# Optimization experiments

Hardware: AMD Instinct MI355X
Metric: run time of the kernel (lower is better)

The kernel has to match this reference:

```python
import jax, jax.numpy as jnp
import numpy as np

N_NODES = 100000
N_EDGES = 1600000
N_FEAT = 8
N_EFEAT = 4
STATE = 32  # node_state_size
N_GEN = 10000
ITERS = 3


def _fix_max(m):
    # TF unsorted_segment_max fills empty segments with dtype.min (finite)
    return jnp.where(jnp.isneginf(m), jnp.finfo(m.dtype).min, m)


def _fix_min(m):
    return jnp.where(jnp.isposinf(m), jnp.finfo(m.dtype).max, m)


def _l2_normalize(x, eps=1e-12):
    return x * jax.lax.rsqrt(jnp.maximum(jnp.sum(x * x, axis=-1, keepdims=True), eps))


def _dense_init(key, fan_in, fan_out):
    return jax.random.normal(key, (fan_in, fan_out), jnp.float32) * (1.0 / np.sqrt(fan_in))


def setup_inputs() -> dict:
    key = jax.random.key(0)
    ks = jax.random.split(key, 12)
    x = jax.random.normal(ks[0], (N_NODES, N_FEAT), jnp.float32)
    edge_weights = jax.random.uniform(ks[1], (N_EDGES, N_EFEAT), jnp.float32)
    edges = jax.random.randint(ks[2], (2, N_EDGES), 0, N_NODES)
    generators_nodes = jax.random.randint(ks[3], (N_GEN,), 0, N_NODES)
    # update_fn: 128 -> 256 -> 128 -> 32 (tanh)
    Wu1 = _dense_init(ks[4], 4 * STATE, 256); bu1 = jnp.zeros((256,), jnp.float32)
    Wu2 = _dense_init(ks[5], 256, 128);       bu2 = jnp.zeros((128,), jnp.float32)
    Wu3 = _dense_init(ks[6], 128, STATE);     bu3 = jnp.zeros((STATE,), jnp.float32)
    # readout: 32 -> 64 -> 32 -> 1 (tanh, tanh, linear)
    Wr1 = _dense_init(ks[7], STATE, 64);      br1 = jnp.zeros((64,), jnp.float32)
    Wr2 = _dense_init(ks[8], 64, 32);         br2 = jnp.zeros((32,), jnp.float32)
    Wr3 = _dense_init(ks[9], 32, 1);          br3 = jnp.zeros((1,), jnp.float32)
    return {"x": x, "edge_weights": edge_weights,
            "Wu1": Wu1, "bu1": bu1, "Wu2": Wu2, "bu2": bu2, "Wu3": Wu3, "bu3": bu3,
            "Wr1": Wr1, "br1": br1, "Wr2": Wr2, "br2": br2, "Wr3": Wr3, "br3": br3,
            "edges": edges, "generators_nodes": generators_nodes}


def reference(x, edge_weights, Wu1, bu1, Wu2, bu2, Wu3, bu3,
              Wr1, br1, Wr2, br2, Wr3, br3, edges, generators_nodes):
    n = x.shape[0]
    node_idx, nbr_idx = edges[0], edges[1]
    ones = jnp.ones((edge_weights.shape[0], 1), x.dtype)
    cnt = jnp.maximum(jax.ops.segment_sum(ones, node_idx, num_segments=n), 1.0)  # [n,1]

    # prepare(): edge-weight stats per destination node, concat with features, pad to STATE
    w_sum = jax.ops.segment_sum(edge_weights, node_idx, num_segments=n)
    w_mean = w_sum / cnt
    w_max = _fix_max(jax.ops.segment_max(edge_weights, node_idx, num_segments=n))
    w_min = _fix_min(jax.ops.segment_min(edge_weights, node_idx, num_segments=n))
    reps = jnp.concatenate([x, w_mean, w_max, w_min, w_sum], axis=1)  # [n, 24]
    reps = jnp.pad(reps, ((0, 0), (0, STATE - reps.shape[1])))        # [n, 32]

    for _ in range(ITERS):
        msgs = jnp.take(reps, nbr_idx, axis=0)  # gather neighbour states [E, 32]
        m_mean = jax.ops.segment_sum(msgs, node_idx, num_segments=n) / cnt
        m_max = _fix_max(jax.ops.segment_max(msgs, node_idx, num_segments=n))
        m_min = _fix_min(jax.ops.segment_min(msgs, node_idx, num_segments=n))
        h = jnp.concatenate([reps, m_mean, m_max, m_min], axis=1)  # [n, 128]
        h = jnp.tanh(h @ Wu1 + bu1)
        h = jnp.tanh(h @ Wu2 + bu2)
        h = jnp.tanh(h @ Wu3 + bu3)
        reps = _l2_normalize(h)

    reps = jnp.where(jnp.isnan(reps), jnp.zeros_like(reps), reps)
    g = jnp.take(reps, generators_nodes, axis=0)  # [n_gen, 32]
    g = jnp.tanh(g @ Wr1 + br1)
    g = jnp.tanh(g @ Wr2 + br2)
    values = g @ Wr3 + br3  # linear final activation
    return values.reshape(-1)
```

## Files before the change

kernel.cpp:

```cpp
#include <hip/hip_runtime.h>
#include <cfloat>
#include <cmath>


typedef _Float16 half_t;
typedef _Float16 half8 __attribute__((ext_vector_type(8)));
typedef _Float16 half4_t __attribute__((ext_vector_type(4)));
typedef _Float16 half2_t __attribute__((ext_vector_type(2)));
typedef float f32x4 __attribute__((ext_vector_type(4)));

#define NPB 512
#define BIN_CAP 9216
#define IDXCAP 4352

__device__ __forceinline__ float fast_tanh(float x) {
    float e = __builtin_amdgcn_exp2f(x * 2.8853900817779268f);
    return 1.0f - 2.0f * __builtin_amdgcn_rcpf(1.0f + e);
}

__device__ __forceinline__ half_t cvt_clamp(float v) {
    return (half_t)fminf(fmaxf(v, -60000.f), 60000.f);
}

__device__ __forceinline__ half2_t h2shfl_xor(half2_t v, int mask) {
    int i = __builtin_bit_cast(int, v);
    i = __shfl_xor(i, mask);
    return __builtin_bit_cast(half2_t, i);
}

__global__ __launch_bounds__(256) void k_binA(
    const int* __restrict__ dst, const int* __restrict__ src,
    const float4* __restrict__ ew4,
    int* __restrict__ binCnt, int4* __restrict__ staged, int E, int nbins) {
    __shared__ int cnt[256], base[256], cur[256];
    int t = threadIdx.x;
    cnt[t] = 0;
    cur[t] = 0;
    __syncthreads();
    int e0 = blockIdx.x * 8192;
#pragma unroll 4
    for (int i = 0; i < 32; ++i) {
        int e = e0 + i * 256 + t;
        if (e < E) atomicAdd(&cnt[dst[e] >> 9], 1);
    }
    __syncthreads();
    if (t < nbins && cnt[t] > 0) base[t] = atomicAdd(&binCnt[t], cnt[t]);
    __syncthreads();
#pragma unroll 4
    for (int i = 0; i < 32; ++i) {
        int e = e0 + i * 256 + t;
        if (e < E) {
            int d = dst[e];
            int b = d >> 9;
            int j = base[b] + atomicAdd(&cur[b], 1);
            if (j < BIN_CAP) {
                float4 w = ew4[e];
                half2_t lo = {(half_t)w.x, (half_t)w.y};
                half2_t hi = {(half_t)w.z, (half_t)w.w};
                staged[(size_t)b * BIN_CAP + j] =
                    make_int4(src[e], d & (NPB - 1),
                              __builtin_bit_cast(int, lo),
                              __builtin_bit_cast(int, hi));
            }
        }
    }
}

__global__ void k_scanN(const int* __restrict__ binCnt, int* __restrict__ binStart,
                        int* __restrict__ row_start, int nbins, int n, int E) {
    __shared__ int sh[256];
    int t = threadIdx.x;
    int v = (t < nbins) ? binCnt[t] : 0;
    sh[t] = v;
    __syncthreads();
    for (int s = 1; s < 256; s <<= 1) {
        int u = (t >= s) ? sh[t - s] : 0;
        __syncthreads();
        sh[t] += u;
        __syncthreads();
    }
    if (t < nbins) binStart[t] = sh[t] - v;
    if (t == 0) row_start[n] = E;
}

__global__ __launch_bounds__(512) void k_binB(
    const int* __restrict__ binCnt, const int* __restrict__ binStart,
    const int4* __restrict__ staged, const float* __restrict__ x,
    int* __restrict__ row_start, int* __restrict__ snbr, int2* __restrict__ sew,
    half_t* __restrict__ reps, int n) {
    __shared__ int deg[NPB], cur[NPB], rsl[NPB];
    int t = threadIdx.x;
    int bin = blockIdx.x;
    int cntE = min(binCnt[bin], BIN_CAP);
    int pbase = binStart[bin];
    const int4* st = staged + (size_t)bin * BIN_CAP;

    deg[t] = 0;
    cur[t] = 0;
    __syncthreads();

    for (int i = t; i < cntE; i += 512)
        atomicAdd(&deg[st[i].y], 1);
    __syncthreads();

    int own = deg[t];
    for (int s = 1; s < NPB; s <<= 1) {
        int u = (t >= s) ? deg[t - s] : 0;
        __syncthreads();
        deg[t] += u;
        __syncthreads();
    }
    int excl = deg[t] - own;
    rsl[t] = pbase + excl;
    int node = bin * NPB + t;
    if (node < n) row_start[node] = pbase + excl;
    __syncthreads();

    for (int i = t; i < cntE; i += 512) {
        int4 v = st[i];
        int p = rsl[v.y] + atomicAdd(&cur[v.y], 1);
        snbr[p] = v.x;
        sew[p] = make_int2(v.z, v.w);
    }
    __syncthreads();

    if (node < n) {
        int base = rsl[t];
        float s0 = 0.f, s1 = 0.f, s2 = 0.f, s3 = 0.f;
        half2_t mxlo = {(half_t)-65504.f, (half_t)-65504.f};
        half2_t mxhi = mxlo;
        half2_t mnlo = {(half_t)65504.f, (half_t)65504.f};
        half2_t mnhi = mnlo;
#pragma unroll 2
        for (int k = 0; k < own; ++k) {
            int2 e = sew[base + k];
            half2_t lo = __builtin_bit_cast(half2_t, e.x);
            half2_t hi = __builtin_bit_cast(half2_t, e.y);
            s0 += (float)lo[0];
            s1 += (float)lo[1];
            s2 += (float)hi[0];
            s3 += (float)hi[1];
            mxlo = __builtin_elementwise_max(mxlo, lo);
            mxhi = __builtin_elementwise_max(mxhi, hi);
            mnlo = __builtin_elementwise_min(mnlo, lo);
            mnhi = __builtin_elementwise_min(mnhi, hi);
        }
        float cnt = fmaxf((float)own, 1.0f);
        float rc = __builtin_amdgcn_rcpf(cnt);
        float mx0, mx1, mx2, mx3, mn0, mn1, mn2, mn3;
        if (own == 0) {
            mx0 = mx1 = mx2 = mx3 = -FLT_MAX;
            mn0 = mn1 = mn2 = mn3 = FLT_MAX;
        } else {
            mx0 = (float)mxlo[0]; mx1 = (float)mxlo[1];
            mx2 = (float)mxhi[0]; mx3 = (float)mxhi[1];
            mn0 = (float)mnlo[0]; mn1 = (float)mnlo[1];
            mn2 = (float)mnhi[0]; mn3 = (float)mnhi[1];
        }
        const float4* x4 = reinterpret_cast<const float4*>(x);
        float4 x0 = x4[node * 2 + 0], x1 = x4[node * 2 + 1];
        half_t* o = &reps[(size_t)node * 32];
        half8 c0 = {cvt_clamp(x0.x), cvt_clamp(x0.y), cvt_clamp(x0.z), cvt_clamp(x0.w),
                    cvt_clamp(x1.x), cvt_clamp(x1.y), cvt_clamp(x1.z), cvt_clamp(x1.w)};
        half8 c1 = {cvt_clamp(s0 * rc), cvt_clamp(s1 * rc), cvt_clamp(s2 * rc), cvt_clamp(s3 * rc),
                    cvt_clamp(mx0), cvt_clamp(mx1), cvt_clamp(mx2), cvt_clamp(mx3)};
        half8 c2 = {cvt_clamp(mn0), cvt_clamp(mn1), cvt_clamp(mn2), cvt_clamp(mn3),
                    cvt_clamp(s0), cvt_clamp(s1), cvt_clamp(s2), cvt_clamp(s3)};
        half8 c3 = {(half_t)0.f, (half_t)0.f, (half_t)0.f, (half_t)0.f,
                    (half_t)0.f, (half_t)0.f, (half_t)0.f, (half_t)0.f};
        *(half8*)&o[0] = c0;
        *(half8*)&o[8] = c1;
        *(half8*)&o[16] = c2;
        *(half8*)&o[24] = c3;
    }
}

__global__ void k_wprep(const float* __restrict__ Wu1, const float* __restrict__ Wu2,
                        const float* __restrict__ Wu3, half_t* __restrict__ Wt1,
                        half_t* __restrict__ Wt2, half_t* __restrict__ Wt3) {
    int i = blockIdx.x * 256 + threadIdx.x;
    if (i < 32768) {
        int nrow = i >> 7, k = i & 127;
        Wt1[i] = (half_t)Wu1[k * 256 + nrow];
    } else if (i < 65536) {
        int j = i - 32768;
        int nrow = j >> 8, k = j & 255;
        Wt2[j] = (half_t)Wu2[k * 128 + nrow];
    } else if (i < 69632) {
        int j = i - 65536;
        int nrow = j >> 7, k = j & 127;
        Wt3[j] = (half_t)Wu3[k * 32 + nrow];
    }
}

#define MFMA16(a, b, c) __builtin_amdgcn_mfma_f32_16x16x32_f16((a), (b), (c), 0, 0, 0)

__global__ __launch_bounds__(512, 6) void k_mlp(
    const half_t* __restrict__ reps_in,
    const int* __restrict__ row_start, const int* __restrict__ snbr,
    const half_t* __restrict__ Wt1, const half_t* __restrict__ Wt2,
    const half_t* __restrict__ Wt3,
    const float* __restrict__ bu1, const float* __restrict__ bu2,
    const float* __restrict__ bu3,
    half_t* __restrict__ reps_out, int n) {
    __shared__ half_t sH[64 * 136];
    __shared__ half_t sh1c[64 * 136];
    __shared__ int sDeg[64], sPerm[64];
    int* sIdx = (int*)sh1c;

    const int tid = threadIdx.x;
    const int w   = tid >> 6;
    const int l15 = tid & 15;
    const int lk  = (tid & 63) >> 4;
    const int node0 = blockIdx.x * 64;

    const int nodeEnd = min(node0 + 64, n);
    const int d0blk = row_start[node0];
    const int ecnt = row_start[nodeEnd] - d0blk;
    const bool lds_ok = (ecnt <= IDXCAP);
    if (tid < 64) {
        int node = node0 + tid;
        sDeg[tid] = (node < n) ? (row_start[node + 1] - row_start[node]) : 0;
    }
    if (lds_ok) {
        for (int i = tid; i < ecnt; i += 512)
            sIdx[i] = __builtin_nontemporal_load(&snbr[d0blk + i]);
    }
    __syncthreads();
    if (tid < 64) {
        int dg = sDeg[tid];
        int rank = 0;
#pragma unroll
        for (int j = 0; j < 64; ++j) {
            int dj = sDeg[j];
            rank += (dj > dg) || (dj == dg && j < tid);
        }
        sPerm[rank] = tid;
    }
    __syncthreads();

    {
        const int sg = tid >> 4;
        const int l  = tid & 15;
        const int nb = l >> 2;
        const int ch = l & 3;

        for (int i = 0; i < 2; ++i) {
            int nl = sPerm[i * 32 + sg];
            int node = node0 + nl;
            float s[8];
            half2_t mx2[4], mn2[4];
#pragma unroll
            for (int f = 0; f < 8; ++f) s[f] = 0.f;
#pragma unroll
            for (int f = 0; f < 4; ++f) {
                mx2[f] = (half2_t){(half_t)-65504.f, (half_t)-65504.f};
                mn2[f] = (half2_t){(half_t)65504.f, (half_t)65504.f};
            }
            int d0 = 0, d1 = 0;
            if (node < n) { d0 = row_start[node]; d1 = row_start[node + 1]; }

            for (int e = d0; e < d1; e += 16) {
                int e0 = e + nb, e1 = e + 4 + nb, e2 = e + 8 + nb, e3 = e + 12 + nb;
                float m0 = (e0 < d1) ? 1.f : 0.f;
                float m1 = (e1 < d1) ? 1.f : 0.f;
                float m2 = (e2 < d1) ? 1.f : 0.f;
                float m3 = (e3 < d1) ? 1.f : 0.f;
                int ii0, ii1, ii2, ii3;
                if (lds_ok) {
                    ii0 = sIdx[min(e0, d1 - 1) - d0blk];
                    ii1 = sIdx[min(e1, d1 - 1) - d0blk];
                    ii2 = sIdx[min(e2, d1 - 1) - d0blk];
                    ii3 = sIdx[min(e3, d1 - 1) - d0blk];
                } else {
                    ii0 = snbr[min(e0, d1 - 1)];
                    ii1 = snbr[min(e1, d1 - 1)];
                    ii2 = snbr[min(e2, d1 - 1)];
                    ii3 = snbr[min(e3, d1 - 1)];
                }
                half8 r0 = *(const half8*)&reps_in[(size_t)ii0 * 32 + ch * 8];
                half8 r1 = *(const half8*)&reps_in[(size_t)ii1 * 32 + ch * 8];
                half8 r2 = *(const half8*)&reps_in[(size_t)ii2 * 32 + ch * 8];
                half8 r3 = *(const half8*)&reps_in[(size_t)ii3 * 32 + ch * 8];
#pragma unroll
                for (int f = 0; f < 4; ++f) {
                    half2_t a0 = (half2_t){r0[2 * f], r0[2 * f + 1]};
                    half2_t a1 = (half2_t){r1[2 * f], r1[2 * f + 1]};
                    half2_t a2 = (half2_t){r2[2 * f], r2[2 * f + 1]};
                    half2_t a3 = (half2_t){r3[2 * f], r3[2 * f + 1]};
                    mx2[f] = __builtin_elementwise_max(
                        __builtin_elementwise_max(mx2[f], a0),
                        __builtin_elementwise_max(a1,
                            __builtin_elementwise_max(a2, a3)));
                    mn2[f] = __builtin_elementwise_min(
                        __builtin_elementwise_min(mn2[f], a0),
                        __builtin_elementwise_min(a1,
                            __builtin_elementwise_min(a2, a3)));
                }
#pragma unroll
                for (int f = 0; f < 8; ++f) {
                    s[f] = fmaf((float)r0[f], m0, s[f]);
                    s[f] = fmaf((float)r1[f], m1, s[f]);
                    s[f] = fmaf((float)r2[f], m2, s[f]);
                    s[f] = fmaf((float)r3[f], m3, s[f]);
                }
            }
#pragma unroll
            for (int f = 0; f < 8; ++f) {
                s[f] += __shfl_xor(s[f], 4);
                s[f] += __shfl_xor(s[f], 8);
            }
#pragma unroll
            for (int f = 0; f < 4; ++f) {
                mx2[f] = __builtin_elementwise_max(mx2[f], h2shfl_xor(mx2[f], 4));
                mx2[f] = __builtin_elementwise_max(mx2[f], h2shfl_xor(mx2[f], 8));
                mn2[f] = __builtin_elementwise_min(mn2[f], h2shfl_xor(mn2[f], 4));
                mn2[f] = __builtin_elementwise_min(mn2[f], h2shfl_xor(mn2[f], 8));
            }
            float cnt = fmaxf((float)(d1 - d0), 1.f);
            half8 o;
            if (nb == 0) {
                if (node < n) {
                    o = *(const half8*)&reps_in[(size_t)node * 32 + ch * 8];
                } else {
#pragma unroll
                    for (int f = 0; f < 8; ++f) o[f] = (half_t)0.f;
                }
            } else if (nb == 1) {
                float rc = __builtin_amdgcn_rcpf(cnt);
#pragma unroll
                for (int f = 0; f < 8; ++f) o[f] = cvt_clamp(s[f] * rc);
            } else if (nb == 2) {
#pragma unroll
                for (int f = 0; f < 4; ++f) {
                    o[2 * f]     = cvt_clamp((float)mx2[f][0]);
                    o[2 * f + 1] = cvt_clamp((float)mx2[f][1]);
                }
            } else {
#pragma unroll
                for (int f = 0; f < 4; ++f) {
                    o[2 * f]     = cvt_clamp((float)mn2[f][0]);
                    o[2 * f + 1] = cvt_clamp((float)mn2[f][1]);
                }
            }
            *(half8*)&sH[nl * 136 + l * 8] = o;
        }
    }
    __syncthreads();

    f32x4 acc2[4] = {{0.f, 0.f, 0.f, 0.f}, {0.f, 0.f, 0.f, 0.f},
                     {0.f, 0.f, 0.f, 0.f}, {0.f, 0.f, 0.f, 0.f}};
#pragma unroll
    for (int c = 0; c < 2; ++c) {
        {
            half8 a[4];
#pragma unroll
            for (int ks = 0; ks < 4; ++ks)
                a[ks] = *(const half8*)&Wt1[(c * 128 + w * 16 + l15) * 128 + ks * 32 + lk * 8];
            f32x4 bv = *(const f32x4*)&bu1[c * 128 + w * 16 + lk * 4];
#pragma unroll
            for (int nt = 0; nt < 4; ++nt) {
                const half_t* hrow = &sH[(nt * 16 + l15) * 136 + lk * 8];
                half8 b0 = *(const half8*)&hrow[0];
                half8 b1 = *(const half8*)&hrow[32];
                half8 b2 = *(const half8*)&hrow[64];
                half8 b3 = *(const half8*)&hrow[96];
                f32x4 acc = {0.f, 0.f, 0.f, 0.f};
                acc = MFMA16(a[0], b0, acc);
                acc = MFMA16(a[1], b1, acc);
                acc = MFMA16(a[2], b2, acc);
                acc = MFMA16(a[3], b3, acc);
                half4_t o;
#pragma unroll
                for (int r = 0; r < 4; ++r)
                    o[r] = (half_t)fast_tanh(acc[r] + bv[r]);
                *(half4_t*)&sh1c[(nt * 16 + l15) * 136 + w * 16 + lk * 4] = o;
            }
        }
        __syncthreads();
        {
            half8 a[4];
#pragma unroll
            for (int ks = 0; ks < 4; ++ks)
                a[ks] = *(const half8*)&Wt2[(w * 16 + l15) * 256 + c * 128 + ks * 32 + lk * 8];
#pragma unroll
            for (int nt = 0; nt < 4; ++nt) {
#pragma unroll
                for (int ks = 0; ks < 4; ++ks) {
                    half8 b = *(const half8*)&sh1c[(nt * 16 + l15) * 136 + ks * 32 + lk * 8];
                    acc2[nt] = MFMA16(a[ks], b, acc2[nt]);
                }
            }
        }
        __syncthreads();
    }

    {
        f32x4 bv = *(const f32x4*)&bu2[w * 16 + lk * 4];
#pragma unroll
        for (int nt = 0; nt < 4; ++nt) {
            half4_t o;
#pragma unroll
            for (int r = 0; r < 4; ++r)
                o[r] = (half_t)fast_tanh(acc2[nt][r] + bv[r]);
            *(half4_t*)&sH[(nt * 16 + l15) * 136 + w * 16 + lk * 4] = o;
        }
    }
    __syncthreads();

    if (w < 4) {
        half8 a0[4], a1[4], b[4];
#pragma unroll
        for (int ks = 0; ks < 4; ++ks) {
            a0[ks] = *(const half8*)&Wt3[l15 * 128 + ks * 32 + lk * 8];
            a1[ks] = *(const half8*)&Wt3[(16 + l15) * 128 + ks * 32 + lk * 8];
            b[ks]  = *(const half8*)&sH[(w * 16 + l15) * 136 + ks * 32 + lk * 8];
        }
        f32x4 acc0 = {0.f, 0.f, 0.f, 0.f}, acc1 = {0.f, 0.f, 0.f, 0.f};
#pragma unroll
        for (int ks = 0; ks < 4; ++ks) {
            acc0 = MFMA16(a0[ks], b[ks], acc0);
            acc1 = MFMA16(a1[ks], b[ks], acc1);
        }
        f32x4 bv0 = *(const f32x4*)&bu3[lk * 4];
        f32x4 bv1 = *(const f32x4*)&bu3[16 + lk * 4];
        float v0[4], v1[4];
        float ss = 0.f;
#pragma unroll
        for (int r = 0; r < 4; ++r) {
            v0[r] = fast_tanh(acc0[r] + bv0[r]);
            v1[r] = fast_tanh(acc1[r] + bv1[r]);
            ss += v0[r] * v0[r] + v1[r] * v1[r];
        }
        ss += __shfl_xor(ss, 16);
        ss += __shfl_xor(ss, 32);
        float sc = rsqrtf(fmaxf(ss, 1e-12f));
        int node = node0 + w * 16 + l15;
        if (node < n) {
            half4_t o0, o1;
#pragma unroll
            for (int r = 0; r < 4; ++r) {
                o0[r] = (half_t)(v0[r] * sc);
                o1[r] = (half_t)(v1[r] * sc);
            }
            *(half4_t*)&reps_out[(size_t)node * 32 + lk * 4] = o0;
            *(half4_t*)&reps_out[(size_t)node * 32 + 16 + lk * 4] = o1;
        }
    }
}

__global__ __launch_bounds__(256) void k_readout(
    const half_t* __restrict__ reps, const int* __restrict__ gen,
    const float* __restrict__ Wr1, const float* __restrict__ br1,
    const float* __restrict__ Wr2, const float* __restrict__ br2,
    const float* __restrict__ Wr3, const float* __restrict__ br3,
    float* __restrict__ out, int ngen) {
    __shared__ float sW1[32 * 64];
    __shared__ float sW2[64 * 32];
    __shared__ float sb1[64];
    __shared__ float sb2[32];
    __shared__ float sW3r[32];
    __shared__ float sb3;
    int tid = threadIdx.x;
    for (int i = tid; i < 2048; i += 256) sW1[i] = Wr1[i];
    for (int i = tid; i < 2048; i += 256) sW2[i] = Wr2[i];
    if (tid < 64) sb1[tid] = br1[tid];
    if (tid < 32) sb2[tid] = br2[tid];
    if (tid < 32) sW3r[tid] = Wr3[tid];
    if (tid == 0) sb3 = br3[0];
    __syncthreads();
    int ig = blockIdx.x * 256 + tid;
    if (ig >= ngen) return;
    int node = gen[ig];
    float g[32];
#pragma unroll
    for (int q = 0; q < 4; ++q) {
        half8 v = *(const half8*)&reps[(size_t)node * 32 + q * 8];
#pragma unroll
        for (int r = 0; r < 8; ++r) {
            float f = (float)v[r];
            g[q * 8 + r] = (f != f) ? 0.f : f;
        }
    }
    float a[64];
#pragma unroll
    for (int o = 0; o < 64; ++o) {
        float acc = sb1[o];
#pragma unroll
        for (int k = 0; k < 32; ++k) acc = fmaf(g[k], sW1[k * 64 + o], acc);
        a[o] = fast_tanh(acc);
    }
    float b[32];
#pragma unroll
    for (int o = 0; o < 32; ++o) {
        float acc = sb2[o];
#pragma unroll
        for (int k = 0; k < 64; ++k) acc = fmaf(a[k], sW2[k * 32 + o], acc);
        b[o] = fast_tanh(acc);
    }
    float acc = sb3;
#pragma unroll
    for (int k = 0; k < 32; ++k) acc = fmaf(b[k], sW3r[k], acc);
    out[ig] = acc;
}

extern "C" void kernel_launch(void* const* d_in, const int* in_sizes, int n_in,
                              void* d_out, int out_size, void* d_ws, size_t ws_size,
                              hipStream_t stream) {
    const float* x   = (const float*)d_in[0];
    const float* ew  = (const float*)d_in[1];
    const float* Wu1 = (const float*)d_in[2];
    const float* bu1 = (const float*)d_in[3];
    const float* Wu2 = (const float*)d_in[4];
    const float* bu2 = (const float*)d_in[5];
    const float* Wu3 = (const float*)d_in[6];
    const float* bu3 = (const float*)d_in[7];
    const float* Wr1 = (const float*)d_in[8];
    const float* br1 = (const float*)d_in[9];
    const float* Wr2 = (const float*)d_in[10];
    const float* br2 = (const float*)d_in[11];
    const float* Wr3 = (const float*)d_in[12];
    const float* br3 = (const float*)d_in[13];
    const int* edges = (const int*)d_in[14];
    const int* gen   = (const int*)d_in[15];

    const int n    = in_sizes[0] / 8;
    const int E    = in_sizes[1] / 4;
    const int ngen = in_sizes[15];
    const int* dst = edges;
    const int* src = edges + E;
    float* out = (float*)d_out;

    const int nblk  = (n + 63) / 64;
    const int npad  = nblk * 64;
    const int nbins = (n + NPB - 1) / NPB;

    char* ws = (char*)d_ws;
    size_t off = 0;
    auto alloc = [&](size_t bytes) -> char* {
        char* p = ws + off;
        off = (off + bytes + 255) & ~(size_t)255;
        return p;
    };
    int* row_start = (int*)alloc((size_t)(n + 1) * 4);
    int* binCnt    = (int*)alloc(256 * 4);
    int* binStart  = (int*)alloc(256 * 4);
    int* snbr      = (int*)alloc((size_t)E * 4);
    int2* sew      = (int2*)alloc((size_t)E * 8);
    half_t* repsA  = (half_t*)alloc((size_t)npad * 32 * 2);
    half_t* repsB  = (half_t*)alloc((size_t)npad * 32 * 2);
    half_t* Wt1    = (half_t*)alloc(32768 * 2);
    half_t* Wt2    = (half_t*)alloc(32768 * 2);
    half_t* Wt3    = (half_t*)alloc(4096 * 2);
    int4* staged   = (int4*)alloc((size_t)nbins * BIN_CAP * 16);

    hipMemsetAsync(binCnt, 0, 256 * 4, stream);
    int nblkA = (E + 8191) / 8192;
    k_binA<<<nblkA, 256, 0, stream>>>(dst, src, (const float4*)ew, binCnt, staged, E, nbins);
    k_scanN<<<1, 256, 0, stream>>>(binCnt, binStart, row_start, nbins, n, E);
    k_binB<<<nbins, 512, 0, stream>>>(binCnt, binStart, staged, x,
                                      row_start, snbr, sew, repsA, n);
    k_wprep<<<272, 256, 0, stream>>>(Wu1, Wu2, Wu3, Wt1, Wt2, Wt3);

    half_t* cur = repsA;
    half_t* nxt = repsB;
    for (int it = 0; it < 3; ++it) {
        k_mlp<<<nblk, 512, 0, stream>>>(cur, row_start, snbr, Wt1, Wt2, Wt3,
                                        bu1, bu2, bu3, nxt, n);
        half_t* t = cur; cur = nxt; nxt = t;
    }

    k_readout<<<(ngen + 255) / 256, 256, 0, stream>>>(cur, gen, Wr1, br1, Wr2, br2,
                                                      Wr3, br3, out, ngen);
}
```

Measured before the change: 307.9 us.

## Compute final message-passing iteration only for generator nodes

The last k_mlp launch now processes only the nodes listed in generators_nodes via an indirection list, instead of all nodes. Only those nodes feed the readout, so the rest of the final iteration's gather and MLP work is dropped. The kernel gains a node-list path that skips the LDS neighbour-index prefetch, so the generator blocks read neighbour indices from global memory with scattered access.

```diff
diff --git a/kernel.cpp b/kernel.cpp
--- a/kernel.cpp
+++ b/kernel.cpp
@@ -198,6 +198,7 @@
 __global__ __launch_bounds__(512, 6) void k_mlp(
     const half_t* __restrict__ reps_in,
     const int* __restrict__ row_start, const int* __restrict__ snbr,
+    const int* __restrict__ nlist, int nlen,
     const half_t* __restrict__ Wt1, const half_t* __restrict__ Wt2,
     const half_t* __restrict__ Wt3,
     const float* __restrict__ bu1, const float* __restrict__ bu2,
@@ -205,7 +206,7 @@
     half_t* __restrict__ reps_out, int n) {
     __shared__ half_t sH[64 * 136];
     __shared__ half_t sh1c[64 * 136];
-    __shared__ int sDeg[64], sPerm[64];
+    __shared__ int sDeg[64], sPerm[64], sNode[64];
     int* sIdx = (int*)sh1c;
 
     const int tid = threadIdx.x;
@@ -214,17 +215,29 @@
     const int lk  = (tid & 63) >> 4;
     const int node0 = blockIdx.x * 64;
 
+    if (tid < 64) {
+        int node;
+        if (nlist) {
+            int li = node0 + tid;
+            node = (li < nlen) ? nlist[li] : -1;
+        } else {
+            node = node0 + tid;
+        }
+        if ((unsigned)node >= (unsigned)n) node = -1;
+        sNode[tid] = node;
+        sDeg[tid] = (node >= 0) ? (row_start[node + 1] - row_start[node]) : 0;
+    }
     const int nodeEnd = min(node0 + 64, n);
-    const int d0blk = row_start[node0];
-    const int ecnt = row_start[nodeEnd] - d0blk;
-    const bool lds_ok = (ecnt <= IDXCAP);
-    if (tid < 64) {
-        int node = node0 + tid;
-        sDeg[tid] = (node < n) ? (row_start[node + 1] - row_start[node]) : 0;
-    }
-    if (lds_ok) {
-        for (int i = tid; i < ecnt; i += 512)
-            sIdx[i] = __builtin_nontemporal_load(&snbr[d0blk + i]);
+    int d0blk = 0;
+    bool lds_ok = false;
+    if (!nlist && node0 < n) {
+        d0blk = row_start[node0];
+        int ecnt = row_start[nodeEnd] - d0blk;
+        lds_ok = (ecnt <= IDXCAP);
+        if (lds_ok) {
+            for (int i = tid; i < ecnt; i += 512)
+                sIdx[i] = __builtin_nontemporal_load(&snbr[d0blk + i]);
+        }
     }
     __syncthreads();
     if (tid < 64) {
@@ -247,7 +260,7 @@
 
         for (int i = 0; i < 2; ++i) {
             int nl = sPerm[i * 32 + sg];
-            int node = node0 + nl;
+            int node = sNode[nl];
             float s[8];
             half2_t mx2[4], mn2[4];
 #pragma unroll
@@ -258,7 +271,7 @@
                 mn2[f] = (half2_t){(half_t)65504.f, (half_t)65504.f};
             }
             int d0 = 0, d1 = 0;
-            if (node < n) { d0 = row_start[node]; d1 = row_start[node + 1]; }
+            if (node >= 0) { d0 = row_start[node]; d1 = row_start[node + 1]; }
 
             for (int e = d0; e < d1; e += 16) {
                 int e0 = e + nb, e1 = e + 4 + nb, e2 = e + 8 + nb, e3 = e + 12 + nb;
@@ -320,7 +333,7 @@
             float cnt = fmaxf((float)(d1 - d0), 1.f);
             half8 o;
             if (nb == 0) {
-                if (node < n) {
+                if (node >= 0) {
                     o = *(const half8*)&reps_in[(size_t)node * 32 + ch * 8];
                 } else {
 #pragma unroll
@@ -435,8 +448,8 @@
         ss += __shfl_xor(ss, 16);
         ss += __shfl_xor(ss, 32);
         float sc = rsqrtf(fmaxf(ss, 1e-12f));
-        int node = node0 + w * 16 + l15;
-        if (node < n) {
+        int node = sNode[w * 16 + l15];
+        if (node >= 0) {
             half4_t o0, o1;
 #pragma unroll
             for (int r = 0; r < 4; ++r) {
@@ -562,14 +575,14 @@
                                       row_start, snbr, sew, repsA, n);
     k_wprep<<<272, 256, 0, stream>>>(Wu1, Wu2, Wu3, Wt1, Wt2, Wt3);
 
-    half_t* cur = repsA;
-    half_t* nxt = repsB;
-    for (int it = 0; it < 3; ++it) {
-        k_mlp<<<nblk, 512, 0, stream>>>(cur, row_start, snbr, Wt1, Wt2, Wt3,
-                                        bu1, bu2, bu3, nxt, n);
-        half_t* t = cur; cur = nxt; nxt = t;
-    }
-
-    k_readout<<<(ngen + 255) / 256, 256, 0, stream>>>(cur, gen, Wr1, br1, Wr2, br2,
+    k_mlp<<<nblk, 512, 0, stream>>>(repsA, row_start, snbr, nullptr, 0,
+                                    Wt1, Wt2, Wt3, bu1, bu2, bu3, repsB, n);
+    k_mlp<<<nblk, 512, 0, stream>>>(repsB, row_start, snbr, nullptr, 0,
+                                    Wt1, Wt2, Wt3, bu1, bu2, bu3, repsA, n);
+    int nblk3 = (ngen + 63) / 64;
+    k_mlp<<<nblk3, 512, 0, stream>>>(repsA, row_start, snbr, gen, ngen,
+                                     Wt1, Wt2, Wt3, bu1, bu2, bu3, repsB, n);
+
+    k_readout<<<(ngen + 255) / 256, 256, 0, stream>>>(repsB, gen, Wr1, br1, Wr2, br2,
                                                       Wr3, br3, out, ngen);
 }
```

Result: faster. 261.8 us, median of 2 (-15.0%).
